# Performance work log

Measured on AMD Instinct MI355X. Metric: run time of the kernel, lower is better.

## Reference

```python
import jax, jax.numpy as jnp
import numpy as np

B, S, E, H = 32, 256, 768, 32
D = E // H  # head_dim = 24


def setup_inputs() -> dict:
    key = jax.random.key(0)
    ks = jax.random.split(key, 10)
    w_sc = 1.0 / np.sqrt(E)  # xavier-ish init scale for weights
    return {
        "feats": jax.random.normal(ks[0], (B, S, E), jnp.float32),
        "attn_bias": jax.random.normal(ks[1], (B, H, S, S), jnp.float32),
        "delta_pos": jax.random.normal(ks[2], (B, S, S, 3), jnp.float32),
        "Wq": jax.random.normal(ks[3], (E, E), jnp.float32) * w_sc,
        "bq": jnp.zeros((E,), jnp.float32),
        "Wk": jax.random.normal(ks[4], (E, E), jnp.float32) * w_sc,
        "bk": jnp.zeros((E,), jnp.float32),
        "Wv": jax.random.normal(ks[5], (E, E), jnp.float32) * w_sc,
        "bv": jnp.zeros((E,), jnp.float32),
        "Wfx": jax.random.normal(ks[6], (E,), jnp.float32) * w_sc,
        "Wfy": jax.random.normal(ks[7], (E,), jnp.float32) * w_sc,
        "Wfz": jax.random.normal(ks[8], (E,), jnp.float32) * w_sc,
    }


def reference(feats, attn_bias, delta_pos, Wq, bq, Wk, bk, Wv, bv, Wfx, Wfy, Wfz):
    b, s, e = feats.shape
    h = attn_bias.shape[1]
    d = e // h
    scaling = d ** -0.5
    # q/k/v projections; q scaled by 1/sqrt(head_dim)
    q = ((feats @ Wq + bq) * scaling).reshape(b, s, h, d).transpose(0, 2, 1, 3)  # (b,h,s,d)
    k = (feats @ Wk + bk).reshape(b, s, h, d).transpose(0, 2, 1, 3)              # (b,h,t,d)
    v = (feats @ Wv + bv).reshape(b, s, h, d).transpose(0, 2, 1, 3)              # (b,h,t,d)
    scores = jnp.einsum('bhsd,bhtd->bhst', q, k) + attn_bias
    probs = jax.nn.softmax(scores, axis=-1)  # dropout p in eval -> identity
    # rot_attn_probs = probs[...,None] * delta_pos[:,None] fused into one contraction:
    # (b,h,s,t) * (b,s,t,3) contracted with (b,h,t,c) over t -> (b,s,3,h,c)
    attn = jnp.einsum('bhst,bstx,bhtc->bsxhc', probs, delta_pos, v)
    attn = attn.reshape(b, s, 3, e)  # flatten (h,c) -> e
    out_x = attn[..., 0, :] @ Wfx  # (b,s)
    out_y = attn[..., 1, :] @ Wfy
    out_z = attn[..., 2, :] @ Wfz
    return jnp.stack([out_x, out_y, out_z], axis=-1)  # (b,s,3)
```

## Files before the change

kernel.cpp:

```cpp
#include <hip/hip_runtime.h>
#include <hip/hip_bf16.h>

#define B_ 32
#define S_ 256
#define E_ 768
#define H_ 32
#define D_ 24
#define NTOT 1664
#define LK 40

typedef __hip_bfloat16 bf16;
typedef __attribute__((ext_vector_type(8))) short short8;
typedef __attribute__((ext_vector_type(4))) float floatx4;
typedef __attribute__((ext_vector_type(2))) float f32x2;

__global__ __launch_bounds__(256) void cast_feats(
    const float* __restrict__ in, bf16* __restrict__ outp, int n4)
{
  int i = blockIdx.x * 256 + threadIdx.x;
  if (i < n4) {
    float4 v = reinterpret_cast<const float4*>(in)[i];
    union { ushort4 u; bf16 b[4]; } pk;
    pk.b[0] = (bf16)v.x; pk.b[1] = (bf16)v.y;
    pk.b[2] = (bf16)v.z; pk.b[3] = (bf16)v.w;
    reinterpret_cast<ushort4*>(outp)[i] = pk.u;
  }
}

__global__ __launch_bounds__(256) void prep_qk(
    const float* __restrict__ Wq, const float* __restrict__ Wk,
    bf16* __restrict__ Wt)
{
  __shared__ float tile[64][65];
  int n0 = blockIdx.x * 64;
  int k0 = blockIdx.y * 64;
  int j = threadIdx.x & 63, i4 = threadIdx.x >> 6;
  const float qscale = 0.20412414523193154f;
  bool isq = (n0 < 768);
  const float* W = isq ? Wq : Wk;
  int nc = isq ? n0 : n0 - 768;
  float sc = isq ? qscale : 1.0f;
  #pragma unroll
  for (int r = 0; r < 16; r++) {
    int i = r * 4 + i4;
    tile[i][j] = W[(size_t)(k0 + i) * E_ + nc + j] * sc;
  }
  __syncthreads();
  #pragma unroll
  for (int r = 0; r < 16; r++) {
    int jj = r * 4 + i4;
    Wt[(size_t)(n0 + jj) * E_ + k0 + j] = (bf16)tile[j][jj];
  }
}

__global__ __launch_bounds__(256) void prep_vw_bias(
    const float* __restrict__ Wv,
    const float* __restrict__ bq, const float* __restrict__ bk,
    const float* __restrict__ bv,
    const float* __restrict__ Wfx, const float* __restrict__ Wfy,
    const float* __restrict__ Wfz,
    bf16* __restrict__ Wt, float* __restrict__ biasf)
{
  const float qscale = 0.20412414523193154f;
  int gid = blockIdx.x * 256 + threadIdx.x;
  if (gid < 128 * E_) {
    int n = 1536 + gid / E_, k = gid % E_;
    float val = 0.f;
    if (n < 1632) {
      int nn = n - 1536, x = nn >> 5, h = nn & 31;
      const float* Wf = (x == 0) ? Wfx : (x == 1 ? Wfy : Wfz);
      #pragma unroll
      for (int c = 0; c < D_; c++)
        val += Wv[(size_t)k * E_ + h * D_ + c] * Wf[h * D_ + c];
    }
    Wt[(size_t)n * E_ + k] = (bf16)val;
  } else {
    int n = gid - 128 * E_;
    if (n < NTOT) {
      float val;
      if (n < 768) {
        val = bq[n] * qscale;
      } else if (n < 1536) {
        val = bk[n - 768];
      } else if (n < 1632) {
        int nn = n - 1536, x = nn >> 5, h = nn & 31;
        const float* Wf = (x == 0) ? Wfx : (x == 1 ? Wfy : Wfz);
        float s = 0.f;
        #pragma unroll
        for (int c = 0; c < D_; c++)
          s += bv[h * D_ + c] * Wf[h * D_ + c];
        val = s;
      } else {
        val = 0.f;
      }
      biasf[n] = val;
    }
  }
}

__global__ __launch_bounds__(256) void gemm_qkv(
    const bf16* __restrict__ A, const bf16* __restrict__ Wt,
    const float* __restrict__ biasf,
    bf16* __restrict__ qout, bf16* __restrict__ kout,
    float* __restrict__ vwout)
{
  __shared__ __align__(16) short As[128 * LK];
  __shared__ __align__(16) short Bs[128 * LK];
  int tid = threadIdx.x;
  int m0 = blockIdx.y * 128, n0 = blockIdx.x * 128;
  int lrow = tid >> 2, lcol = (tid & 3) * 8;
  int wave = tid >> 6, lane = tid & 63;
  int wm = (wave >> 1) * 64, wn = (wave & 1) * 64;
  int fr = lane & 15, quad = lane >> 4;

  floatx4 acc[4][4];
  const floatx4 zero = {0.f, 0.f, 0.f, 0.f};
  #pragma unroll
  for (int i = 0; i < 4; i++)
    #pragma unroll
    for (int j = 0; j < 4; j++) acc[i][j] = zero;

  const bf16* Aptr = A + (size_t)(m0 + lrow) * E_ + lcol;
  const bf16* Bptr = Wt + (size_t)(n0 + lrow) * E_ + lcol;
  float4 av0 = *reinterpret_cast<const float4*>(Aptr);
  float4 av1 = *reinterpret_cast<const float4*>(Aptr + (size_t)64 * E_);
  float4 bv0 = *reinterpret_cast<const float4*>(Bptr);
  float4 bv1 = *reinterpret_cast<const float4*>(Bptr + (size_t)64 * E_);

  for (int k0 = 0; k0 < E_; k0 += 32) {
    __syncthreads();
    *reinterpret_cast<float4*>(&As[lrow * LK + lcol]) = av0;
    *reinterpret_cast<float4*>(&As[(lrow + 64) * LK + lcol]) = av1;
    *reinterpret_cast<float4*>(&Bs[lrow * LK + lcol]) = bv0;
    *reinterpret_cast<float4*>(&Bs[(lrow + 64) * LK + lcol]) = bv1;
    __syncthreads();
    if (k0 + 32 < E_) {
      av0 = *reinterpret_cast<const float4*>(Aptr + k0 + 32);
      av1 = *reinterpret_cast<const float4*>(Aptr + (size_t)64 * E_ + k0 + 32);
      bv0 = *reinterpret_cast<const float4*>(Bptr + k0 + 32);
      bv1 = *reinterpret_cast<const float4*>(Bptr + (size_t)64 * E_ + k0 + 32);
    }
    short8 af[4], bfr[4];
    #pragma unroll
    for (int t = 0; t < 4; t++)
      af[t] = *reinterpret_cast<const short8*>(
          &As[(wm + t * 16 + fr) * LK + quad * 8]);
    #pragma unroll
    for (int t = 0; t < 4; t++)
      bfr[t] = *reinterpret_cast<const short8*>(
          &Bs[(wn + t * 16 + fr) * LK + quad * 8]);
    #pragma unroll
    for (int ti = 0; ti < 4; ti++)
      #pragma unroll
      for (int tj = 0; tj < 4; tj++)
        acc[ti][tj] = __builtin_amdgcn_mfma_f32_16x16x32_bf16(
            af[ti], bfr[tj], acc[ti][tj], 0, 0, 0);
  }

  #pragma unroll
  for (int ti = 0; ti < 4; ti++) {
    #pragma unroll
    for (int tj = 0; tj < 4; tj++) {
      int n = n0 + wn + tj * 16 + fr;
      float bias = biasf[n];
      #pragma unroll
      for (int r = 0; r < 4; r++) {
        int m = m0 + wm + ti * 16 + quad * 4 + r;
        int b = m >> 8, s = m & 255;
        float val = acc[ti][tj][r] + bias;
        if (n < 768) {
          qout[(size_t)(b * S_ + s) * E_ + n] = (bf16)val;
        } else if (n < 1536) {
          kout[(size_t)(b * S_ + s) * E_ + (n - 768)] = (bf16)val;
        } else if (n < 1632) {
          int nn = n - 1536, x = nn >> 5, hh = nn & 31;
          vwout[(((size_t)x * B_ + b) * H_ + hh) * S_ + s] = val;
        }
      }
    }
  }
}

__global__ __launch_bounds__(256) void attn_kernel(
    const bf16* __restrict__ qg, const bf16* __restrict__ kg,
    const float* __restrict__ vwg, const float* __restrict__ biasg,
    const float* __restrict__ dpg, float* __restrict__ part)
{
  __shared__ __align__(16) float ql[64 * 26];
  int blk = blockIdx.x;
  int b = blk & 31;
  int u = blk >> 5;
  int h = u & 31;
  int st = (u >> 5) * 64;
  int bh = b * H_ + h;
  int tid = threadIdx.x, wave = tid >> 6, lane = tid & 63;
  int t0 = lane * 4;

  f32x2 kr[4][12];
  #pragma unroll
  for (int j = 0; j < 4; j++) {
    const short8* kp = reinterpret_cast<const short8*>(
        kg + (size_t)(b * S_ + t0 + j) * E_ + h * D_);
    #pragma unroll
    for (int seg = 0; seg < 3; seg++) {
      short8 kk = kp[seg];
      #pragma unroll
      for (int p2 = 0; p2 < 4; p2++) {
        union { short u; bf16 bb; } a, c;
        a.u = kk[2 * p2]; c.u = kk[2 * p2 + 1];
        f32x2 t2; t2.x = (float)a.bb; t2.y = (float)c.bb;
        kr[j][seg * 4 + p2] = t2;
      }
    }
  }
  float vwr[3][4];
  #pragma unroll
  for (int x = 0; x < 3; x++) {
    float4 v4 = *reinterpret_cast<const float4*>(
        vwg + (((size_t)x * B_ + b) * H_ + h) * S_ + t0);
    vwr[x][0] = v4.x; vwr[x][1] = v4.y; vwr[x][2] = v4.z; vwr[x][3] = v4.w;
  }
  {
    int r = tid >> 2, c0 = (tid & 3) * 6;
    const bf16* qrow = qg + (size_t)(b * S_ + st + r) * E_ + h * D_ + c0;
    #pragma unroll
    for (int i = 0; i < 6; i++) ql[r * 26 + c0 + i] = (float)qrow[i];
  }
  __syncthreads();

  const float* biasbh = biasg + (size_t)bh * S_ * S_;
  const float* dpb    = dpg + (size_t)b * S_ * S_ * 3;

  float4 pb[2], pe0[2], pe1[2], pe2[2];
  #pragma unroll
  for (int w = 0; w < 2; w++) {
    int s0 = st + w * 4 + wave;
    pb[w] = *reinterpret_cast<const float4*>(biasbh + (size_t)s0 * S_ + t0);
    const float* dpr = dpb + (size_t)s0 * S_ * 3 + (size_t)t0 * 3;
    pe0[w] = *reinterpret_cast<const float4*>(dpr);
    pe1[w] = *reinterpret_cast<const float4*>(dpr + 4);
    pe2[w] = *reinterpret_cast<const float4*>(dpr + 8);
  }

  #pragma unroll
  for (int si = 0; si < 16; si++) {
    const int cur = si & 1;
    float4 bias4 = pb[cur], e0 = pe0[cur], e1 = pe1[cur], e2 = pe2[cur];
    int nsi = (si + 2 < 16) ? si + 2 : 0;
    int ns = st + nsi * 4 + wave;
    pb[cur] = *reinterpret_cast<const float4*>(biasbh + (size_t)ns * S_ + t0);
    const float* dpn = dpb + (size_t)ns * S_ * 3 + (size_t)t0 * 3;
    pe0[cur] = *reinterpret_cast<const float4*>(dpn);
    pe1[cur] = *reinterpret_cast<const float4*>(dpn + 4);
    pe2[cur] = *reinterpret_cast<const float4*>(dpn + 8);

    int sr = si * 4 + wave;
    int s  = st + sr;

    f32x2 sc2[4];
    #pragma unroll
    for (int j = 0; j < 4; j++) { sc2[j].x = 0.f; sc2[j].y = 0.f; }
    #pragma unroll
    for (int i = 0; i < 12; i++) {
      f32x2 qd = *reinterpret_cast<const f32x2*>(&ql[sr * 26 + 2 * i]);
      #pragma unroll
      for (int j = 0; j < 4; j++) sc2[j] += qd * kr[j][i];
    }
    float p[4];
    p[0] = __expf(sc2[0].x + sc2[0].y + bias4.x - 4.0f);
    p[1] = __expf(sc2[1].x + sc2[1].y + bias4.y - 4.0f);
    p[2] = __expf(sc2[2].x + sc2[2].y + bias4.z - 4.0f);
    p[3] = __expf(sc2[3].x + sc2[3].y + bias4.w - 4.0f);
    float l = (p[0] + p[1]) + (p[2] + p[3]);

    float dx[4] = {e0.x, e0.w, e1.z, e2.y};
    float dy[4] = {e0.y, e1.x, e1.w, e2.z};
    float dz[4] = {e0.z, e1.y, e2.x, e2.w};

    float ax = 0.f, ay = 0.f, az = 0.f;
    #pragma unroll
    for (int j = 0; j < 4; j++) {
      ax = fmaf(p[j] * dx[j], vwr[0][j], ax);
      ay = fmaf(p[j] * dy[j], vwr[1][j], ay);
      az = fmaf(p[j] * dz[j], vwr[2][j], az);
    }
    #pragma unroll
    for (int o = 32; o; o >>= 1) {
      ax += __shfl_xor(ax, o);
      ay += __shfl_xor(ay, o);
      az += __shfl_xor(az, o);
      l  += __shfl_xor(l, o);
    }
    if (lane == 0) {
      float inv = 1.0f / l;
      float* op = part + ((size_t)bh * S_ + s) * 3;
      op[0] = ax * inv; op[1] = ay * inv; op[2] = az * inv;
    }
  }
}

__global__ __launch_bounds__(256) void reduce_h(
    const float* __restrict__ part, float* __restrict__ out)
{
  int k = blockIdx.x * 256 + threadIdx.x;
  int b = k / (S_ * 3);
  int r = k - b * (S_ * 3);
  const float* p = part + (size_t)b * H_ * S_ * 3 + r;
  float acc = 0.f;
  #pragma unroll
  for (int h = 0; h < H_; h++) acc += p[(size_t)h * S_ * 3];
  out[k] = acc;
}

extern "C" void kernel_launch(void* const* d_in, const int* in_sizes, int n_in,
                              void* d_out, int out_size, void* d_ws, size_t ws_size,
                              hipStream_t stream)
{
  const float* feats     = (const float*)d_in[0];
  const float* attn_bias = (const float*)d_in[1];
  const float* delta_pos = (const float*)d_in[2];
  const float* Wq        = (const float*)d_in[3];
  const float* bq        = (const float*)d_in[4];
  const float* Wk        = (const float*)d_in[5];
  const float* bk        = (const float*)d_in[6];
  const float* Wv        = (const float*)d_in[7];
  const float* bv        = (const float*)d_in[8];
  const float* Wfx       = (const float*)d_in[9];
  const float* Wfy       = (const float*)d_in[10];
  const float* Wfz       = (const float*)d_in[11];

  char* ws = (char*)d_ws;
  size_t off = 0;
  auto alloc = [&](size_t bytes) -> void* {
    void* p = ws + off;
    off = (off + bytes + 255) & ~(size_t)255;
    return p;
  };
  bf16*  ws_fb   = (bf16*) alloc((size_t)B_ * S_ * E_ * 2);
  bf16*  ws_q    = (bf16*) alloc((size_t)B_ * S_ * E_ * 2);
  bf16*  ws_k    = (bf16*) alloc((size_t)B_ * S_ * E_ * 2);
  float* ws_vw   = (float*)alloc((size_t)3 * B_ * H_ * S_ * 4);
  bf16*  ws_Wt   = (bf16*) alloc((size_t)NTOT * E_ * 2);
  float* ws_bias = (float*)alloc((size_t)NTOT * 4);
  float* ws_part = (float*)alloc((size_t)B_ * H_ * S_ * 3 * 4);

  int n4 = B_ * S_ * E_ / 4;
  cast_feats<<<(n4 + 255) / 256, 256, 0, stream>>>(feats, ws_fb, n4);

  prep_qk<<<dim3(24, 12), 256, 0, stream>>>(Wq, Wk, ws_Wt);

  int prep_n = 128 * E_ + NTOT;
  prep_vw_bias<<<(prep_n + 255) / 256, 256, 0, stream>>>(
      Wv, bq, bk, bv, Wfx, Wfy, Wfz, ws_Wt, ws_bias);

  gemm_qkv<<<dim3(NTOT / 128, B_ * S_ / 128), 256, 0, stream>>>(
      ws_fb, ws_Wt, ws_bias, ws_q, ws_k, ws_vw);

  attn_kernel<<<B_ * H_ * 4, 256, 0, stream>>>(ws_q, ws_k, ws_vw, attn_bias,
                                               delta_pos, ws_part);

  reduce_h<<<(B_ * S_ * 3) / 256, 256, 0, stream>>>(ws_part, (float*)d_out);
}
```

Before: 537.7 us.

## Load GEMM tiles directly to LDS with XOR swizzle; shallower attention prefetch

The QKV GEMM now stages A and B tiles with global_load_lds DMA into an unpadded, XOR-swizzled LDS layout, replacing the register-staged loads and the padded rows. This removes register traffic and the padding, but it also drops the overlap of next-tile global loads with MFMA compute, since loads are now issued and waited on in the same iteration. Separately, the attention kernel's bias/delta_pos prefetch goes from two rows ahead to one and the loop is no longer fully unrolled, which is meant to lower register pressure.

```diff
diff --git a/kernel.cpp b/kernel.cpp
--- a/kernel.cpp
+++ b/kernel.cpp
@@ -7,12 +7,16 @@
 #define H_ 32
 #define D_ 24
 #define NTOT 1664
-#define LK 40
 
 typedef __hip_bfloat16 bf16;
 typedef __attribute__((ext_vector_type(8))) short short8;
 typedef __attribute__((ext_vector_type(4))) float floatx4;
 typedef __attribute__((ext_vector_type(2))) float f32x2;
+
+#define GLOAD_LDS16(g, l)                                          \
+  __builtin_amdgcn_global_load_lds(                                \
+      (const __attribute__((address_space(1))) void*)(g),          \
+      (__attribute__((address_space(3))) void*)(l), 16, 0, 0)
 
 __global__ __launch_bounds__(256) void cast_feats(
     const float* __restrict__ in, bf16* __restrict__ outp, int n4)
@@ -104,15 +108,21 @@
     bf16* __restrict__ qout, bf16* __restrict__ kout,
     float* __restrict__ vwout)
 {
-  __shared__ __align__(16) short As[128 * LK];
-  __shared__ __align__(16) short Bs[128 * LK];
+  __shared__ __align__(16) short As[128 * 32];
+  __shared__ __align__(16) short Bs[128 * 32];
   int tid = threadIdx.x;
   int m0 = blockIdx.y * 128, n0 = blockIdx.x * 128;
-  int lrow = tid >> 2, lcol = (tid & 3) * 8;
   int wave = tid >> 6, lane = tid & 63;
   int wm = (wave >> 1) * 64, wn = (wave & 1) * 64;
   int fr = lane & 15, quad = lane >> 4;
 
+  int srow = wave * 32 + (lane >> 2);
+  int schunk = (lane & 3) ^ (srow & 3);
+  const bf16* Asrc = A + (size_t)(m0 + srow) * E_ + schunk * 8;
+  const bf16* Bsrc = Wt + (size_t)(n0 + srow) * E_ + schunk * 8;
+  short* AsW = As + wave * 1024;
+  short* BsW = Bs + wave * 1024;
+
   floatx4 acc[4][4];
   const floatx4 zero = {0.f, 0.f, 0.f, 0.f};
   #pragma unroll
@@ -120,35 +130,29 @@
     #pragma unroll
     for (int j = 0; j < 4; j++) acc[i][j] = zero;
 
-  const bf16* Aptr = A + (size_t)(m0 + lrow) * E_ + lcol;
-  const bf16* Bptr = Wt + (size_t)(n0 + lrow) * E_ + lcol;
-  float4 av0 = *reinterpret_cast<const float4*>(Aptr);
-  float4 av1 = *reinterpret_cast<const float4*>(Aptr + (size_t)64 * E_);
-  float4 bv0 = *reinterpret_cast<const float4*>(Bptr);
-  float4 bv1 = *reinterpret_cast<const float4*>(Bptr + (size_t)64 * E_);
+  int ra[4], rb[4];
+  #pragma unroll
+  for (int t = 0; t < 4; t++) {
+    int rowa = wm + t * 16 + fr;
+    int rowb = wn + t * 16 + fr;
+    ra[t] = rowa * 32 + (quad ^ (rowa & 3)) * 8;
+    rb[t] = rowb * 32 + (quad ^ (rowb & 3)) * 8;
+  }
 
   for (int k0 = 0; k0 < E_; k0 += 32) {
+    if (k0) __syncthreads();
+    GLOAD_LDS16(Asrc + k0, AsW);
+    GLOAD_LDS16(Asrc + (size_t)16 * E_ + k0, AsW + 512);
+    GLOAD_LDS16(Bsrc + k0, BsW);
+    GLOAD_LDS16(Bsrc + (size_t)16 * E_ + k0, BsW + 512);
     __syncthreads();
-    *reinterpret_cast<float4*>(&As[lrow * LK + lcol]) = av0;
-    *reinterpret_cast<float4*>(&As[(lrow + 64) * LK + lcol]) = av1;
-    *reinterpret_cast<float4*>(&Bs[lrow * LK + lcol]) = bv0;
-    *reinterpret_cast<float4*>(&Bs[(lrow + 64) * LK + lcol]) = bv1;
-    __syncthreads();
-    if (k0 + 32 < E_) {
-      av0 = *reinterpret_cast<const float4*>(Aptr + k0 + 32);
-      av1 = *reinterpret_cast<const float4*>(Aptr + (size_t)64 * E_ + k0 + 32);
-      bv0 = *reinterpret_cast<const float4*>(Bptr + k0 + 32);
-      bv1 = *reinterpret_cast<const float4*>(Bptr + (size_t)64 * E_ + k0 + 32);
-    }
     short8 af[4], bfr[4];
     #pragma unroll
     for (int t = 0; t < 4; t++)
-      af[t] = *reinterpret_cast<const short8*>(
-          &As[(wm + t * 16 + fr) * LK + quad * 8]);
+      af[t] = *reinterpret_cast<const short8*>(&As[ra[t]]);
     #pragma unroll
     for (int t = 0; t < 4; t++)
-      bfr[t] = *reinterpret_cast<const short8*>(
-          &Bs[(wn + t * 16 + fr) * LK + quad * 8]);
+      bfr[t] = *reinterpret_cast<const short8*>(&Bs[rb[t]]);
     #pragma unroll
     for (int ti = 0; ti < 4; ti++)
       #pragma unroll
@@ -231,28 +235,25 @@
   const float* biasbh = biasg + (size_t)bh * S_ * S_;
   const float* dpb    = dpg + (size_t)b * S_ * S_ * 3;
 
-  float4 pb[2], pe0[2], pe1[2], pe2[2];
-  #pragma unroll
-  for (int w = 0; w < 2; w++) {
-    int s0 = st + w * 4 + wave;
-    pb[w] = *reinterpret_cast<const float4*>(biasbh + (size_t)s0 * S_ + t0);
+  float4 nb, nd0, nd1, nd2;
+  {
+    int s0 = st + wave;
+    nb = *reinterpret_cast<const float4*>(biasbh + (size_t)s0 * S_ + t0);
     const float* dpr = dpb + (size_t)s0 * S_ * 3 + (size_t)t0 * 3;
-    pe0[w] = *reinterpret_cast<const float4*>(dpr);
-    pe1[w] = *reinterpret_cast<const float4*>(dpr + 4);
-    pe2[w] = *reinterpret_cast<const float4*>(dpr + 8);
-  }
-
-  #pragma unroll
+    nd0 = *reinterpret_cast<const float4*>(dpr);
+    nd1 = *reinterpret_cast<const float4*>(dpr + 4);
+    nd2 = *reinterpret_cast<const float4*>(dpr + 8);
+  }
+
   for (int si = 0; si < 16; si++) {
-    const int cur = si & 1;
-    float4 bias4 = pb[cur], e0 = pe0[cur], e1 = pe1[cur], e2 = pe2[cur];
-    int nsi = (si + 2 < 16) ? si + 2 : 0;
+    float4 bias4 = nb, e0 = nd0, e1 = nd1, e2 = nd2;
+    int nsi = (si + 1 < 16) ? si + 1 : 0;
     int ns = st + nsi * 4 + wave;
-    pb[cur] = *reinterpret_cast<const float4*>(biasbh + (size_t)ns * S_ + t0);
+    nb = *reinterpret_cast<const float4*>(biasbh + (size_t)ns * S_ + t0);
     const float* dpn = dpb + (size_t)ns * S_ * 3 + (size_t)t0 * 3;
-    pe0[cur] = *reinterpret_cast<const float4*>(dpn);
-    pe1[cur] = *reinterpret_cast<const float4*>(dpn + 4);
-    pe2[cur] = *reinterpret_cast<const float4*>(dpn + 8);
+    nd0 = *reinterpret_cast<const float4*>(dpn);
+    nd1 = *reinterpret_cast<const float4*>(dpn + 4);
+    nd2 = *reinterpret_cast<const float4*>(dpn + 8);
 
     int sr = si * 4 + wave;
     int s  = st + sr;
```

Measured after the change: 551.5 us. +2.6%, slower.
